# Kernel optimization log

Hardware: AMD Instinct MI355X
Metric: run time of the kernel (lower is better)

Reference implementation:

```python
import jax, jax.numpy as jnp
import numpy as np

N_NODES = 100000
N_EDGES = 1600000
IN_DIM = 128
HID = 128
OUT = 128
NUM_GRAPHS = 2048


def setup_inputs() -> dict:
    key = jax.random.key(0)
    ks = jax.random.split(key, 10)
    x = jax.random.normal(ks[0], (N_NODES, IN_DIM), dtype=jnp.float32)
    edge_index = jax.random.randint(ks[1], (2, N_EDGES), 0, N_NODES, dtype=jnp.int32)
    graph_index = jnp.sort(jax.random.randint(ks[2], (N_NODES,), 0, NUM_GRAPHS, dtype=jnp.int32))
    def glorot(k, fi, fo):
        lim = jnp.sqrt(6.0 / (fi + fo)).astype(jnp.float32)
        return jax.random.uniform(k, (fi, fo), jnp.float32, -lim, lim)
    return {
        "x": x,
        "edge_index": edge_index,
        "graph_index": graph_index,
        "num_graphs": NUM_GRAPHS,
        "W1": glorot(ks[3], IN_DIM, HID), "b1": jnp.zeros((HID,), jnp.float32),
        "W2": glorot(ks[4], HID, HID),    "b2": jnp.zeros((HID,), jnp.float32),
        "W3": glorot(ks[5], HID, OUT),    "b3": jnp.zeros((OUT,), jnp.float32),
    }


def _gcn_layer(x, src, dst, norm, W, b, n_nodes):
    # transform first (cheap GEMM), then normalized gather-scatter aggregation
    h = x @ W                              # [N, F]
    msg = h[src] * norm[:, None]           # [E+N, F] gather + scale
    out = jax.ops.segment_sum(msg, dst, num_segments=n_nodes)  # scatter-add
    return out + b


def reference(x, edge_index, graph_index, num_graphs, W1, b1, W2, b2, W3, b3):
    n = x.shape[0]
    # add self-loops (PyG GCNConv default)
    loops = jnp.arange(n, dtype=edge_index.dtype)
    src = jnp.concatenate([edge_index[0], loops])
    dst = jnp.concatenate([edge_index[1], loops])
    # symmetric normalization D^-1/2 (A+I) D^-1/2, degree = in-degree incl. self-loop
    deg = jax.ops.segment_sum(jnp.ones_like(src, dtype=x.dtype), dst, num_segments=n)
    dinv = jax.lax.rsqrt(jnp.maximum(deg, 1.0))
    norm = dinv[src] * dinv[dst]
    # 3 conv layers + ReLU (dropout = identity at inference)
    h = jax.nn.relu(_gcn_layer(x, src, dst, norm, W1, b1, n))
    h = jax.nn.relu(_gcn_layer(h, src, dst, norm, W2, b2, n))
    h = jax.nn.relu(_gcn_layer(h, src, dst, norm, W3, b3, n))
    # global mean / max pooling per graph
    gsum = jax.ops.segment_sum(h, graph_index, num_segments=num_graphs)
    cnt = jax.ops.segment_sum(jnp.ones((n,), h.dtype), graph_index, num_segments=num_graphs)
    gmean = gsum / jnp.maximum(cnt, 1.0)[:, None]
    gmax = jax.ops.segment_max(h, graph_index, num_segments=num_graphs)
    return jnp.concatenate([gmean, gmax], axis=-1)
```

## Files before the change

### kernel.cpp

```cpp
#include <hip/hip_runtime.h>
#include <hip/hip_bf16.h>
#include <stdint.h>

#define N_NODES   100000
#define N_EDGES   1600000
#define FDIM      128
#define NUM_GR    2048
#define CSR_CAP   64

#define NBKT      391
#define BKT_CAP   4864
#define TILE      4096
#define LBIN_CAP  16
#define LBIN_STR  17

typedef __attribute__((ext_vector_type(8))) short short8;
typedef __attribute__((ext_vector_type(4))) float f32x4;

__device__ __forceinline__ uint32_t pk2(float a, float b) {
    __hip_bfloat16 x = __float2bfloat16(a), y = __float2bfloat16(b);
    uint16_t ux = *reinterpret_cast<uint16_t*>(&x);
    uint16_t uy = *reinterpret_cast<uint16_t*>(&y);
    return (uint32_t)ux | ((uint32_t)uy << 16);
}

__device__ __forceinline__ float bflo(uint32_t u) { return __uint_as_float(u << 16); }
__device__ __forceinline__ float bfhi(uint32_t u) { return __uint_as_float(u & 0xFFFF0000u); }

__device__ __forceinline__ short8 pack8(float4 u0, float4 u1) {
    union { uint32_t u[4]; short8 s; } cv;
    cv.u[0] = pk2(u0.x, u0.y);
    cv.u[1] = pk2(u0.z, u0.w);
    cv.u[2] = pk2(u1.x, u1.y);
    cv.u[3] = pk2(u1.z, u1.w);
    return cv.s;
}

__device__ __forceinline__ int lower_bound_dev(const int* a, int n, int key) {
    int lo = 0, hi = n;
    while (lo < hi) {
        int m = (lo + hi) >> 1;
        if (a[m] < key) lo = m + 1; else hi = m;
    }
    return lo;
}


__global__ __launch_bounds__(256, 4) void k_fused1(
        const float* __restrict__ x, const float* __restrict__ W1,
        __hip_bfloat16* __restrict__ C, int n, int gGemm,
        const int* __restrict__ src, const int* __restrict__ dst,
        int* __restrict__ bkt_cnt, int* __restrict__ bkt, int E, int gA,
        const float* __restrict__ W2, const float* __restrict__ W3,
        __hip_bfloat16* __restrict__ wt,
        const int* __restrict__ gidx, float* __restrict__ gscale) {
    __shared__ uint32_t smem[8192];
    const int b = blockIdx.x;
    const int tid = threadIdx.x;

    if (b >= gGemm + gA + 128) {
        int g = (b - (gGemm + gA + 128)) * 256 + tid;
        if (g < NUM_GR) {
            int lo = lower_bound_dev(gidx, n, g);
            int hi = lower_bound_dev(gidx, n, g + 1);
            gscale[g] = 1.f / (float)max(hi - lo, 1);
        }
        return;
    }

    if (b >= gGemm + gA) {
        int idx = 16384 + (b - gGemm - gA) * 256 + tid;
        int l = idx >> 14, rem = idx & 16383, c = rem >> 7, k = rem & 127;
        const float* W = (l == 1) ? W2 : W3;
        wt[idx] = __float2bfloat16(W[k * FDIM + c]);
        return;
    }

    if (b >= gGemm) {
        int* binCnt  = (int*)smem;
        int* binBase = (int*)smem + NBKT;
        int* bins    = (int*)smem + 2 * NBKT;
        int bb = b - gGemm;

        for (int i = tid; i < NBKT; i += 256) binCnt[i] = 0;
        __syncthreads();

        int e0 = bb * TILE;
        int e1 = min(E, e0 + TILE);
        for (int e = e0 + tid; e < e1; e += 256) {
            int s = src[e];
            int d = dst[e];
            int bi = d >> 8;
            int rec = ((d & 255) << 17) | s;
            int pos = atomicAdd(&binCnt[bi], 1);
            if (pos < LBIN_CAP) {
                bins[bi * LBIN_STR + pos] = rec;
            } else {
                int gp = atomicAdd(&bkt_cnt[bi], 1);
                if (gp < BKT_CAP) bkt[bi * BKT_CAP + gp] = rec;
            }
        }
        __syncthreads();

        for (int i = tid; i < NBKT; i += 256) {
            int c = min(binCnt[i], LBIN_CAP);
            binBase[i] = (c > 0) ? atomicAdd(&bkt_cnt[i], c) : 0;
        }
        __syncthreads();

        for (int i = tid; i < NBKT * LBIN_CAP; i += 256) {
            int bi = i / LBIN_CAP, sl = i - bi * LBIN_CAP;
            if (sl < min(binCnt[bi], LBIN_CAP)) {
                int gp = binBase[bi] + sl;
                if (gp < BKT_CAP) bkt[bi * BKT_CAP + gp] = bins[bi * LBIN_STR + sl];
            }
        }
        return;
    }

    uint32_t* Wtl = smem;

    const int rowBase = b * 128;

    for (int it = 0; it < 32; ++it) {
        int idx = it * 256 + tid;
        int kp = idx >> 7;
        int c  = idx & 127;
        float w0 = W1[(size_t)(2 * kp) * FDIM + c];
        float w1 = W1[(size_t)(2 * kp + 1) * FDIM + c];
        int word = c * 64 + ((((kp >> 2) ^ (c & 7)) << 2) | (kp & 3));
        Wtl[word] = pk2(w0, w1);
    }
    __syncthreads();

    const int w = tid >> 6;
    const int lane = tid & 63;
    const int r = lane & 15;
    const int q = lane >> 4;

    const int r0c = min(rowBase + w * 32 + r, n - 1);
    const int r1c = min(rowBase + w * 32 + 16 + r, n - 1);

    f32x4 acc[8][2] = {};

#pragma unroll
    for (int kk = 0; kk < 4; ++kk) {
        int co = (kk * 4 + q) * 8;
        const float4* p0 = (const float4*)&x[(size_t)r0c * FDIM + co];
        const float4* p1 = (const float4*)&x[(size_t)r1c * FDIM + co];
        short8 a0 = pack8(p0[0], p0[1]);
        short8 a1 = pack8(p1[0], p1[1]);
        int gr = ((kk * 4 + q) ^ (r & 7)) << 2;
#pragma unroll
        for (int m = 0; m < 8; ++m) {
            short8 bw = *(const short8*)&Wtl[(m * 16 + r) * 64 + gr];
            acc[m][0] = __builtin_amdgcn_mfma_f32_16x16x32_bf16(bw, a0, acc[m][0], 0, 0, 0);
            acc[m][1] = __builtin_amdgcn_mfma_f32_16x16x32_bf16(bw, a1, acc[m][1], 0, 0, 0);
        }
    }

#pragma unroll
    for (int nt = 0; nt < 2; ++nt) {
        int node = rowBase + w * 32 + nt * 16 + r;
        if (node < n) {
#pragma unroll
            for (int m = 0; m < 8; ++m) {
                f32x4 v = acc[m][nt];
                uint2 pv;
                pv.x = pk2(v[0], v[1]);
                pv.y = pk2(v[2], v[3]);
                *(uint2*)&C[(size_t)node * FDIM + m * 16 + q * 4] = pv;
            }
        }
    }
}


__global__ __launch_bounds__(256) void k_csr(const int* __restrict__ bkt_cnt,
                                             const int* __restrict__ bkt,
                                             int* __restrict__ cnt,
                                             float* __restrict__ dinv,
                                             int* __restrict__ csr,
                                             uint32_t* __restrict__ za,
                                             uint32_t* __restrict__ zb,
                                             float* __restrict__ outz,
                                             int n) {
    __shared__ int lc[64];
    __shared__ int cur[64];
    int b = blockIdx.x;
    int tid = threadIdx.x;
    int bi = b >> 2;
    int qd = b & 3;

    if (b == 0) {
        if (tid == 0) dinv[n] = 0.f;
        if (tid < 64) za[(size_t)n * 64 + tid] = 0;
    }
    if (b == 1 && tid < 64) zb[(size_t)n * 64 + tid] = 0;
    for (int i = b * 256 + tid; i < NUM_GR * 256; i += NBKT * 4 * 256)
        outz[i] = 0.f;

    if (tid < 64) { lc[tid] = 0; cur[tid] = 0; }
    __syncthreads();

    int len = min(bkt_cnt[bi], BKT_CAP);
    const int* recs = bkt + bi * BKT_CAP;

    for (int i = tid; i < len; i += 256) {
        int dl = (recs[i] >> 17) & 255;
        if ((dl >> 6) == qd) atomicAdd(&lc[dl & 63], 1);
    }
    __syncthreads();

    if (tid < 64) {
        int v = (bi << 8) + (qd << 6) + tid;
        if (v < n) {
            int c = lc[tid];
            cnt[v] = c;
            dinv[v] = rsqrtf((float)(c + 1));
        }
    }

    for (int i = tid; i < len; i += 256) {
        int rec = recs[i];
        int dl = (rec >> 17) & 255;
        if ((dl >> 6) == qd) {
            int pos = atomicAdd(&cur[dl & 63], 1);
            if (pos < CSR_CAP)
                csr[(((size_t)(bi << 8) + dl) << 6) + pos] = rec & 0x1FFFF;
        }
    }
}


__global__ __launch_bounds__(256) void k_agg1(const __hip_bfloat16* __restrict__ T,
                                              const int* __restrict__ cnt,
                                              const int* __restrict__ csr,
                                              const float* __restrict__ dinv,
                                              const float* __restrict__ bias,
                                              uint32_t* __restrict__ Hb,
                                              int n) {
    int wid = (blockIdx.x * 256 + threadIdx.x) >> 6;
    int lane = threadIdx.x & 63;
    if (wid >= n) return;
    int v = wid;
    int g   = lane >> 4;
    int s16 = lane & 15;

    const uint4* Tu4 = (const uint4*)T;

    int cv  = min(cnt[v], CSR_CAP);
    int sraw = csr[((size_t)v << 6) + lane];
    int sidx = (lane < cv) ? sraw : ((lane == cv) ? v : n);
    cv += 1;

    float a0 = 0.f, a1 = 0.f, a2 = 0.f, a3 = 0.f;
    float a4 = 0.f, a5 = 0.f, a6 = 0.f, a7 = 0.f;

    int mr = (cv + 15) & ~15;
    for (int j = 0; j < mr; j += 16) {
        uint4 gg[4];
        float wv[4];
#pragma unroll
        for (int t = 0; t < 4; ++t) {
            int it = __shfl(sidx, j + 4 * t + g, 64);
            wv[t] = dinv[it];
            gg[t] = Tu4[(size_t)it * 16 + s16];
        }
#pragma unroll
        for (int t = 0; t < 4; ++t) {
            a0 = fmaf(wv[t], bflo(gg[t].x), a0); a1 = fmaf(wv[t], bfhi(gg[t].x), a1);
            a2 = fmaf(wv[t], bflo(gg[t].y), a2); a3 = fmaf(wv[t], bfhi(gg[t].y), a3);
            a4 = fmaf(wv[t], bflo(gg[t].z), a4); a5 = fmaf(wv[t], bfhi(gg[t].z), a5);
            a6 = fmaf(wv[t], bflo(gg[t].w), a6); a7 = fmaf(wv[t], bfhi(gg[t].w), a7);
        }
    }

    a0 += __shfl_xor(a0, 16, 64); a0 += __shfl_xor(a0, 32, 64);
    a1 += __shfl_xor(a1, 16, 64); a1 += __shfl_xor(a1, 32, 64);
    a2 += __shfl_xor(a2, 16, 64); a2 += __shfl_xor(a2, 32, 64);
    a3 += __shfl_xor(a3, 16, 64); a3 += __shfl_xor(a3, 32, 64);
    a4 += __shfl_xor(a4, 16, 64); a4 += __shfl_xor(a4, 32, 64);
    a5 += __shfl_xor(a5, 16, 64); a5 += __shfl_xor(a5, 32, 64);
    a6 += __shfl_xor(a6, 16, 64); a6 += __shfl_xor(a6, 32, 64);
    a7 += __shfl_xor(a7, 16, 64); a7 += __shfl_xor(a7, 32, 64);

    if (g == 0) {
        float dv = dinv[v];
        float4 bb0 = *(const float4*)&bias[s16 * 8];
        float4 bb1 = *(const float4*)&bias[s16 * 8 + 4];
        float r0 = fmaxf(fmaf(dv, a0, bb0.x), 0.f);
        float r1 = fmaxf(fmaf(dv, a1, bb0.y), 0.f);
        float r2 = fmaxf(fmaf(dv, a2, bb0.z), 0.f);
        float r3 = fmaxf(fmaf(dv, a3, bb0.w), 0.f);
        float r4 = fmaxf(fmaf(dv, a4, bb1.x), 0.f);
        float r5 = fmaxf(fmaf(dv, a5, bb1.y), 0.f);
        float r6 = fmaxf(fmaf(dv, a6, bb1.z), 0.f);
        float r7 = fmaxf(fmaf(dv, a7, bb1.w), 0.f);
        uint4 pv;
        pv.x = pk2(r0, r1);
        pv.y = pk2(r2, r3);
        pv.z = pk2(r4, r5);
        pv.w = pk2(r6, r7);
        *(uint4*)&Hb[(size_t)v * 64 + s16 * 4] = pv;
    }
}


template<int POOL>
__global__ __launch_bounds__(512, 4) void k_aggT(
        const __hip_bfloat16* __restrict__ T,
        const __hip_bfloat16* __restrict__ Wt,
        const int* __restrict__ cnt,
        const int* __restrict__ csr,
        const float* __restrict__ dinv,
        const float* __restrict__ bias,
        uint32_t* __restrict__ Hb,
        const int* __restrict__ gidx,
        const float* __restrict__ gscale,
        float* __restrict__ out,
        int n) {
    __shared__ uint32_t Wl[128 * 64];
    __shared__ uint32_t Hl[32 * 64];

    const int tid = threadIdx.x;

    for (int it = 0; it < 4; ++it) {
        int g = it * 512 + tid;
        int r = g >> 4;
        int seg = g & 15;
        uint4 v = *(const uint4*)&Wt[(size_t)r * FDIM + seg * 8];
        int word = r * 64 + ((seg ^ (r & 7)) << 2);
        *(uint4*)&Wl[word] = v;
    }

    const int w = tid >> 6;
    const int lane = tid & 63;
    const int g = lane >> 4;
    const int s16 = lane & 15;
    const int nodeBase = blockIdx.x * 32;
    const uint4* Tu4 = (const uint4*)T;

    for (int k = 0; k < 4; ++k) {
        int v = nodeBase + w * 4 + k;
        int cv = min(cnt[v], CSR_CAP);
        int sraw = csr[((size_t)v << 6) + lane];
        int sidx = (lane < cv) ? sraw : ((lane == cv) ? v : n);
        cv += 1;

        float a0 = 0.f, a1 = 0.f, a2 = 0.f, a3 = 0.f;
        float a4 = 0.f, a5 = 0.f, a6 = 0.f, a7 = 0.f;

        int mr = (cv + 15) & ~15;
        for (int j = 0; j < mr; j += 16) {
            uint4 gg[4];
            float wv[4];
#pragma unroll
            for (int t = 0; t < 4; ++t) {
                int it = __shfl(sidx, j + 4 * t + g, 64);
                wv[t] = dinv[it];
                gg[t] = Tu4[(size_t)it * 16 + s16];
            }
#pragma unroll
            for (int t = 0; t < 4; ++t) {
                a0 = fmaf(wv[t], bflo(gg[t].x), a0); a1 = fmaf(wv[t], bfhi(gg[t].x), a1);
                a2 = fmaf(wv[t], bflo(gg[t].y), a2); a3 = fmaf(wv[t], bfhi(gg[t].y), a3);
                a4 = fmaf(wv[t], bflo(gg[t].z), a4); a5 = fmaf(wv[t], bfhi(gg[t].z), a5);
                a6 = fmaf(wv[t], bflo(gg[t].w), a6); a7 = fmaf(wv[t], bfhi(gg[t].w), a7);
            }
        }

        a0 += __shfl_xor(a0, 16, 64); a0 += __shfl_xor(a0, 32, 64);
        a1 += __shfl_xor(a1, 16, 64); a1 += __shfl_xor(a1, 32, 64);
        a2 += __shfl_xor(a2, 16, 64); a2 += __shfl_xor(a2, 32, 64);
        a3 += __shfl_xor(a3, 16, 64); a3 += __shfl_xor(a3, 32, 64);
        a4 += __shfl_xor(a4, 16, 64); a4 += __shfl_xor(a4, 32, 64);
        a5 += __shfl_xor(a5, 16, 64); a5 += __shfl_xor(a5, 32, 64);
        a6 += __shfl_xor(a6, 16, 64); a6 += __shfl_xor(a6, 32, 64);
        a7 += __shfl_xor(a7, 16, 64); a7 += __shfl_xor(a7, 32, 64);

        if (g == 0) {
            float dv = dinv[v];
            int row = w * 4 + k;
            uint4 pv;
            pv.x = pk2(a0 * dv, a1 * dv);
            pv.y = pk2(a2 * dv, a3 * dv);
            pv.z = pk2(a4 * dv, a5 * dv);
            pv.w = pk2(a6 * dv, a7 * dv);
            *(uint4*)&Hl[row * 64 + ((s16 ^ (row & 7)) << 2)] = pv;
        }
    }
    __syncthreads();

    const int r = lane & 15;
    const int q = lane >> 4;

    f32x4 acc[2] = {};
#pragma unroll
    for (int kk = 0; kk < 4; ++kk) {
        int gr = ((kk * 4 + q) ^ (r & 7)) << 2;
        short8 a0 = *(const short8*)&Hl[r * 64 + gr];
        short8 a1 = *(const short8*)&Hl[(16 + r) * 64 + gr];
        short8 bw = *(const short8*)&Wl[(w * 16 + r) * 64 + gr];
        acc[0] = __builtin_amdgcn_mfma_f32_16x16x32_bf16(bw, a0, acc[0], 0, 0, 0);
        acc[1] = __builtin_amdgcn_mfma_f32_16x16x32_bf16(bw, a1, acc[1], 0, 0, 0);
    }

    float4 bb = *(const float4*)&bias[w * 16 + q * 4];

    if constexpr (!POOL) {
#pragma unroll
        for (int nt = 0; nt < 2; ++nt) {
            int node = nodeBase + nt * 16 + r;
            f32x4 vv = acc[nt];
            float r0 = fmaxf(vv[0] + bb.x, 0.f);
            float r1 = fmaxf(vv[1] + bb.y, 0.f);
            float r2 = fmaxf(vv[2] + bb.z, 0.f);
            float r3 = fmaxf(vv[3] + bb.w, 0.f);
            uint2 pv;
            pv.x = pk2(r0, r1);
            pv.y = pk2(r2, r3);
            *(uint2*)&Hb[(size_t)node * 64 + w * 8 + q * 2] = pv;
        }
    } else {
        __syncthreads();
        float* Pl = (float*)Wl;
        int* lds_g = (int*)Hl;
#pragma unroll
        for (int nt = 0; nt < 2; ++nt) {
            int row = nt * 16 + r;
            f32x4 vv = acc[nt];
            float* dstp = &Pl[row * 130 + w * 16 + q * 4];
            dstp[0] = fmaxf(vv[0] + bb.x, 0.f);
            dstp[1] = fmaxf(vv[1] + bb.y, 0.f);
            dstp[2] = fmaxf(vv[2] + bb.z, 0.f);
            dstp[3] = fmaxf(vv[3] + bb.w, 0.f);
        }
        if (tid < 32) lds_g[tid] = gidx[nodeBase + tid];
        __syncthreads();
        if (tid < 128) {
            int f = tid;
            int cg = lds_g[0];
            float s = 0.f, m = 0.f;
            for (int row = 0; row < 32; ++row) {
                int gw = lds_g[row];
                float hv = Pl[row * 130 + f];
                if (gw != cg) {
                    atomicAdd(&out[(size_t)cg * 256 + f], s * gscale[cg]);
                    atomicMax((unsigned int*)&out[(size_t)cg * 256 + 128 + f],
                              __float_as_uint(m));
                    s = 0.f; m = 0.f; cg = gw;
                }
                s += hv;
                m = fmaxf(m, hv);
            }
            atomicAdd(&out[(size_t)cg * 256 + f], s * gscale[cg]);
            atomicMax((unsigned int*)&out[(size_t)cg * 256 + 128 + f],
                      __float_as_uint(m));
        }
    }
}


extern "C" void kernel_launch(void* const* d_in, const int* in_sizes, int n_in,
                              void* d_out, int out_size, void* d_ws, size_t ws_size,
                              hipStream_t stream) {
    const float* x    = (const float*)d_in[0];
    const int*   ei   = (const int*)d_in[1];
    const int*   gidx = (const int*)d_in[2];
    const float* W1 = (const float*)d_in[4];
    const float* b1 = (const float*)d_in[5];
    const float* W2 = (const float*)d_in[6];
    const float* b2 = (const float*)d_in[7];
    const float* W3 = (const float*)d_in[8];
    const float* b3 = (const float*)d_in[9];
    float* out = (float*)d_out;

    const int N = N_NODES, E = N_EDGES;
    const int* src = ei;
    const int* dst = ei + E;

    char* ws = (char*)d_ws;
    size_t o = 0;
    auto alloc = [&](size_t bytes) { size_t r = o; o += (bytes + 255) & ~(size_t)255; return r; };
    size_t o_bktcnt = alloc((size_t)NBKT * 4);
    size_t o_bkt    = alloc((size_t)NBKT * BKT_CAP * 4);
    size_t o_cnt    = alloc((size_t)N * 4);
    size_t o_dinv   = alloc((size_t)(N + 1) * 4);
    size_t o_csr    = alloc((size_t)NBKT * 256 * CSR_CAP * 4);
    size_t o_wt     = alloc((size_t)3 * FDIM * FDIM * 2);
    size_t o_ta     = alloc((size_t)(N + 1) * FDIM * 2);
    size_t o_tb     = alloc((size_t)(N + 1) * FDIM * 2);
    size_t o_gs     = alloc((size_t)NUM_GR * 4);

    int*   bkt_cnt = (int*)(ws + o_bktcnt);
    int*   bkt     = (int*)(ws + o_bkt);
    int*   cnt     = (int*)(ws + o_cnt);
    float* dinv    = (float*)(ws + o_dinv);
    int*   csr     = (int*)(ws + o_csr);
    __hip_bfloat16* wtbuf = (__hip_bfloat16*)(ws + o_wt);
    __hip_bfloat16* bufA  = (__hip_bfloat16*)(ws + o_ta);
    __hip_bfloat16* bufB  = (__hip_bfloat16*)(ws + o_tb);
    float* gscale = (float*)(ws + o_gs);

    hipMemsetAsync(bkt_cnt, 0, (size_t)NBKT * 4, stream);

    const int gA    = (E + TILE - 1) / TILE;
    const int gGemm = (N + 127) / 128;

    k_fused1<<<gGemm + gA + 128 + 8, 256, 0, stream>>>(x, W1, bufA, N, gGemm,
                                                       src, dst, bkt_cnt, bkt, E, gA,
                                                       W2, W3, wtbuf, gidx, gscale);
    k_csr<<<NBKT * 4, 256, 0, stream>>>(bkt_cnt, bkt, cnt, dinv, csr,
                                        (uint32_t*)bufA, (uint32_t*)bufB, out, N);

    k_agg1<<<(N + 3) / 4, 256, 0, stream>>>(bufA, cnt, csr, dinv, b1,
                                            (uint32_t*)bufB, N);
    k_aggT<0><<<N / 32, 512, 0, stream>>>(bufB, wtbuf + FDIM * FDIM,
                                          cnt, csr, dinv, b2, (uint32_t*)bufA,
                                          nullptr, nullptr, nullptr, N);
    k_aggT<1><<<N / 32, 512, 0, stream>>>(bufA, wtbuf + 2 * FDIM * FDIM,
                                          cnt, csr, dinv, b3, nullptr,
                                          gidx, gscale, out, N);
}
```

Baseline: 362.5 us.

## Let each wave transform its own aggregated rows to drop block barrier

In the non-pooling layer kernel, each wave now runs the MFMA transform only on the 4 node rows it aggregated itself, looping over all 8 output column tiles. This removes the block-wide barrier between aggregation and GEMM, so waves no longer wait on one another; a single barrier after the weight load stays. The cost is redundant MFMA work, since only 4 of 16 rows in each 16x16 tile are useful, which is 4x more matrix instructions and more weight reads from LDS.

```diff
diff --git a/kernel.cpp b/kernel.cpp
--- a/kernel.cpp
+++ b/kernel.cpp
@@ -333,6 +333,7 @@
         int word = r * 64 + ((seg ^ (r & 7)) << 2);
         *(uint4*)&Wl[word] = v;
     }
+    __syncthreads();
 
     const int w = tid >> 6;
     const int lane = tid & 63;
@@ -390,39 +391,56 @@
             *(uint4*)&Hl[row * 64 + ((s16 ^ (row & 7)) << 2)] = pv;
         }
     }
-    __syncthreads();
 
     const int r = lane & 15;
     const int q = lane >> 4;
 
-    f32x4 acc[2] = {};
-#pragma unroll
-    for (int kk = 0; kk < 4; ++kk) {
-        int gr = ((kk * 4 + q) ^ (r & 7)) << 2;
-        short8 a0 = *(const short8*)&Hl[r * 64 + gr];
-        short8 a1 = *(const short8*)&Hl[(16 + r) * 64 + gr];
-        short8 bw = *(const short8*)&Wl[(w * 16 + r) * 64 + gr];
-        acc[0] = __builtin_amdgcn_mfma_f32_16x16x32_bf16(bw, a0, acc[0], 0, 0, 0);
-        acc[1] = __builtin_amdgcn_mfma_f32_16x16x32_bf16(bw, a1, acc[1], 0, 0, 0);
-    }
-
-    float4 bb = *(const float4*)&bias[w * 16 + q * 4];
-
     if constexpr (!POOL) {
-#pragma unroll
-        for (int nt = 0; nt < 2; ++nt) {
-            int node = nodeBase + nt * 16 + r;
-            f32x4 vv = acc[nt];
-            float r0 = fmaxf(vv[0] + bb.x, 0.f);
-            float r1 = fmaxf(vv[1] + bb.y, 0.f);
-            float r2 = fmaxf(vv[2] + bb.z, 0.f);
-            float r3 = fmaxf(vv[3] + bb.w, 0.f);
-            uint2 pv;
-            pv.x = pk2(r0, r1);
-            pv.y = pk2(r2, r3);
-            *(uint2*)&Hb[(size_t)node * 64 + w * 8 + q * 2] = pv;
+        const int row = w * 4 + (r & 3);
+        const int rs = row & 7;
+        short8 av[4];
+#pragma unroll
+        for (int kk = 0; kk < 4; ++kk)
+            av[kk] = *(const short8*)&Hl[row * 64 + (((kk * 4 + q) ^ rs) << 2)];
+
+#pragma unroll
+        for (int m = 0; m < 8; ++m) {
+            f32x4 acc = {};
+#pragma unroll
+            for (int kk = 0; kk < 4; ++kk) {
+                int gr = ((kk * 4 + q) ^ (r & 7)) << 2;
+                short8 bw = *(const short8*)&Wl[(m * 16 + r) * 64 + gr];
+                acc = __builtin_amdgcn_mfma_f32_16x16x32_bf16(bw, av[kk], acc, 0, 0, 0);
+            }
+            if (r < 4) {
+                int node = nodeBase + w * 4 + r;
+                float4 bb = *(const float4*)&bias[m * 16 + q * 4];
+                float r0 = fmaxf(acc[0] + bb.x, 0.f);
+                float r1 = fmaxf(acc[1] + bb.y, 0.f);
+                float r2 = fmaxf(acc[2] + bb.z, 0.f);
+                float r3 = fmaxf(acc[3] + bb.w, 0.f);
+                uint2 pv;
+                pv.x = pk2(r0, r1);
+                pv.y = pk2(r2, r3);
+                *(uint2*)&Hb[(size_t)node * 64 + m * 8 + q * 2] = pv;
+            }
         }
     } else {
+        __syncthreads();
+
+        f32x4 acc[2] = {};
+#pragma unroll
+        for (int kk = 0; kk < 4; ++kk) {
+            int gr = ((kk * 4 + q) ^ (r & 7)) << 2;
+            short8 a0 = *(const short8*)&Hl[r * 64 + gr];
+            short8 a1 = *(const short8*)&Hl[(16 + r) * 64 + gr];
+            short8 bw = *(const short8*)&Wl[(w * 16 + r) * 64 + gr];
+            acc[0] = __builtin_amdgcn_mfma_f32_16x16x32_bf16(bw, a0, acc[0], 0, 0, 0);
+            acc[1] = __builtin_amdgcn_mfma_f32_16x16x32_bf16(bw, a1, acc[1], 0, 0, 0);
+        }
+
+        float4 bb = *(const float4*)&bias[w * 16 + q * 4];
+
         __syncthreads();
         float* Pl = (float*)Wl;
         int* lds_g = (int*)Hl;
```

New measurement: 372.6 us. +2.8%, slower.

## Build padded CSR rows in LDS with self-loop and degree-balance node-to-wave assignment

Applied to the files above, without the earlier changes.

The CSR build kernel now assembles each 64-node slab of neighbour lists in shared memory, pre-filled with the sentinel index and with the self-loop already inserted. It then writes the slab with coalesced 16-byte stores instead of scattered 4-byte writes, so the aggregation kernels no longer need per-lane select logic. In the fused aggregate-transform kernel, the 32 nodes of a block are ranked by degree and dealt to waves in a serpentine pattern to even out per-wave gather work. This adds extra syncs and a small O(32^2) rank computation per block, and caps neighbour lists at 63 instead of 64.

```diff
diff --git a/kernel.cpp b/kernel.cpp
--- a/kernel.cpp
+++ b/kernel.cpp
@@ -187,6 +187,7 @@
                                              int n) {
     __shared__ int lc[64];
     __shared__ int cur[64];
+    __shared__ int rows[64 * 64];
     int b = blockIdx.x;
     int tid = threadIdx.x;
     int bi = b >> 2;
@@ -201,6 +202,7 @@
         outz[i] = 0.f;
 
     if (tid < 64) { lc[tid] = 0; cur[tid] = 0; }
+    for (int i = tid; i < 64 * 64; i += 256) rows[i] = n;
     __syncthreads();
 
     int len = min(bkt_cnt[bi], BKT_CAP);
@@ -218,18 +220,25 @@
             int c = lc[tid];
             cnt[v] = c;
             dinv[v] = rsqrtf((float)(c + 1));
-        }
-    }
+            rows[tid * 64 + min(c, CSR_CAP - 1)] = v;
+        }
+    }
+    __syncthreads();
 
     for (int i = tid; i < len; i += 256) {
         int rec = recs[i];
         int dl = (rec >> 17) & 255;
         if ((dl >> 6) == qd) {
             int pos = atomicAdd(&cur[dl & 63], 1);
-            if (pos < CSR_CAP)
-                csr[(((size_t)(bi << 8) + dl) << 6) + pos] = rec & 0x1FFFF;
-        }
-    }
+            if (pos < CSR_CAP - 1)
+                rows[(dl & 63) * 64 + pos] = rec & 0x1FFFF;
+        }
+    }
+    __syncthreads();
+
+    uint4* dstq = (uint4*)(csr + ((size_t)((bi << 8) + (qd << 6)) << 6));
+    const uint4* srcq = (const uint4*)rows;
+    for (int i = tid; i < 1024; i += 256) dstq[i] = srcq[i];
 }
 
 
@@ -249,10 +258,8 @@
 
     const uint4* Tu4 = (const uint4*)T;
 
-    int cv  = min(cnt[v], CSR_CAP);
-    int sraw = csr[((size_t)v << 6) + lane];
-    int sidx = (lane < cv) ? sraw : ((lane == cv) ? v : n);
-    cv += 1;
+    int sidx = csr[((size_t)v << 6) + lane];
+    int cv = min(cnt[v], CSR_CAP - 1) + 1;
 
     float a0 = 0.f, a1 = 0.f, a2 = 0.f, a3 = 0.f;
     float a4 = 0.f, a5 = 0.f, a6 = 0.f, a7 = 0.f;
@@ -324,6 +331,10 @@
     __shared__ uint32_t Hl[32 * 64];
 
     const int tid = threadIdx.x;
+    const int nodeBase = blockIdx.x * 32;
+
+    int* degl = (int*)Hl;
+    int* perm = (int*)Hl + 32;
 
     for (int it = 0; it < 4; ++it) {
         int g = it * 512 + tid;
@@ -333,20 +344,38 @@
         int word = r * 64 + ((seg ^ (r & 7)) << 2);
         *(uint4*)&Wl[word] = v;
     }
+    if (tid < 32) degl[tid] = cnt[nodeBase + tid];
+    __syncthreads();
+
+    if (tid < 32) {
+        int d = degl[tid];
+        int rank = 0;
+        for (int j = 0; j < 32; ++j) {
+            int dj = degl[j];
+            rank += (dj > d) || (dj == d && j < tid);
+        }
+        int band = rank >> 3, rw = rank & 7;
+        int wv = (band & 1) ? (7 - rw) : rw;
+        perm[wv * 4 + band] = tid;
+    }
+    __syncthreads();
 
     const int w = tid >> 6;
     const int lane = tid & 63;
     const int g = lane >> 4;
     const int s16 = lane & 15;
-    const int nodeBase = blockIdx.x * 32;
     const uint4* Tu4 = (const uint4*)T;
 
+    int nib[4];
+#pragma unroll
+    for (int k = 0; k < 4; ++k) nib[k] = perm[w * 4 + k];
+    __syncthreads();
+
     for (int k = 0; k < 4; ++k) {
-        int v = nodeBase + w * 4 + k;
-        int cv = min(cnt[v], CSR_CAP);
-        int sraw = csr[((size_t)v << 6) + lane];
-        int sidx = (lane < cv) ? sraw : ((lane == cv) ? v : n);
-        cv += 1;
+        int row = nib[k];
+        int v = nodeBase + row;
+        int sidx = csr[((size_t)v << 6) + lane];
+        int cv = min(cnt[v], CSR_CAP - 1) + 1;
 
         float a0 = 0.f, a1 = 0.f, a2 = 0.f, a3 = 0.f;
         float a4 = 0.f, a5 = 0.f, a6 = 0.f, a7 = 0.f;
@@ -381,7 +410,6 @@
 
         if (g == 0) {
             float dv = dinv[v];
-            int row = w * 4 + k;
             uint4 pv;
             pv.x = pk2(a0 * dv, a1 * dv);
             pv.y = pk2(a2 * dv, a3 * dv);
```

Measured after the change: 367.3 us. Within noise of the previous version (+1.3%).
